# Performance work log

Hardware: AMD Instinct MI355X
Metric: run time of the kernel (lower is better)

Reference implementation:

```python
import jax, jax.numpy as jnp
import numpy as np

T, E, D = 16384, 16, 2048
CAPACITY = 2048  # per-expert capacity (supported_capacities=[2048])
TOP_K = 2


def setup_inputs() -> dict:
    key = jax.random.key(0)
    k1, k2, k3 = jax.random.split(key, 3)
    in_flow = jax.random.normal(k1, (T, D), dtype=jnp.float32)
    # router scores and a realistic top-k multi-hot mask
    logits = jax.random.normal(k2, (T, E), dtype=jnp.float32)
    score = jax.nn.softmax(logits, axis=-1)
    _, topk_idx = jax.lax.top_k(logits, TOP_K)  # [T, TOP_K]
    hot_mask = jnp.zeros((T, E), jnp.int32).at[jnp.arange(T)[:, None], topk_idx].set(1)
    return {"in_flow": in_flow, "hot_mask": hot_mask, "score": score}


def reference(in_flow, hot_mask, score):
    """Capacity-based fused MoE dispatch (HomoFusedDispatchSF):
    1) per-expert local indices via column-wise cumsum of the multi-hot mask,
    2) capacity-clipped loads,
    3) gather tokens scaled by gate score into expert-local buffers [E*C, D].
    """
    hm = (hot_mask > 0).astype(jnp.int32)               # [T, E]
    local = jnp.cumsum(hm, axis=0) * hm                 # 1-based local index per (token, expert)
    loads = jnp.minimum(hm.sum(axis=0), CAPACITY)       # [E]
    pos = local - 1                                     # 0-based slot within expert buffer
    valid = (hm > 0) & (pos < CAPACITY)                 # capacity overflow -> token dropped
    sentinel = E * CAPACITY
    dst = jnp.where(valid, jnp.arange(E)[None, :] * CAPACITY + pos, sentinel).reshape(-1)  # [T*E]
    tok = jnp.broadcast_to(jnp.arange(T, dtype=jnp.int32)[:, None], (T, E)).reshape(-1)
    # invert the scatter: which source token feeds each output slot (T = empty)
    src_tok = jnp.full((sentinel + 1,), T, jnp.int32).at[dst].set(tok)[:sentinel]          # [E*C]
    gate = jnp.zeros((sentinel + 1,), score.dtype).at[dst].set(score.reshape(-1))[:sentinel]
    slot_valid = src_tok < T
    gathered = jnp.take(in_flow, jnp.minimum(src_tok, T - 1), axis=0)                      # [E*C, D]
    out = jnp.where(slot_valid[:, None], gathered * gate[:, None], jnp.zeros((), in_flow.dtype))
    return out, loads
```

## Files before the change

### kernel.cpp

```cpp
#include <hip/hip_runtime.h>

#define T_TOK 16384
#define E_EXP 16
#define CAP   2048
#define D_DIM 2048
#define NCHUNK (T_TOK / 256)
#define NZERO  128

typedef float vf4 __attribute__((ext_vector_type(4)));

__global__ __launch_bounds__(256) void count_kernel(
    const int* __restrict__ hot_mask,
    int*       __restrict__ counts)
{
    const int chunk = blockIdx.x;
    const int tid   = threadIdx.x;
    const int t     = chunk * 256 + tid;
    const int lane  = tid & 63;
    const int wv    = tid >> 6;

    const int4* row = (const int4*)(hot_mask + (size_t)t * E_EXP);
    int4 r0 = row[0], r1 = row[1], r2 = row[2], r3 = row[3];
    int hm[16] = { r0.x > 0, r0.y > 0, r0.z > 0, r0.w > 0,
                   r1.x > 0, r1.y > 0, r1.z > 0, r1.w > 0,
                   r2.x > 0, r2.y > 0, r2.z > 0, r2.w > 0,
                   r3.x > 0, r3.y > 0, r3.z > 0, r3.w > 0 };

    __shared__ int wcnt[4][16];
    #pragma unroll
    for (int e = 0; e < 16; ++e) {
        unsigned long long m = __ballot(hm[e]);
        if (lane == 0) wcnt[wv][e] = __popcll(m);
    }
    __syncthreads();
    if (tid < 16)
        counts[chunk * E_EXP + tid] =
            wcnt[0][tid] + wcnt[1][tid] + wcnt[2][tid] + wcnt[3][tid];
}

__global__ __launch_bounds__(256) void scanfill_kernel(
    const int*   __restrict__ hot_mask,
    const float* __restrict__ score,
    const int*   __restrict__ counts,
    int*         __restrict__ dst2,
    float*       __restrict__ g2,
    int*         __restrict__ loads_i,
    float*       __restrict__ loads_out)
{
    const int chunk = blockIdx.x;
    const int tid   = threadIdx.x;
    const int t     = chunk * 256 + tid;
    const int lane  = tid & 63;
    const int wv    = tid >> 6;

    __shared__ int s_off[16];
    __shared__ int wcnt[4][16];

    if (tid < 16) {
        const int e = tid;
        int off = 0, tot = 0;
        #pragma unroll 8
        for (int c = 0; c < NCHUNK; ++c) {
            const int v = counts[c * E_EXP + e];
            off += (c < chunk) ? v : 0;
            tot += v;
        }
        s_off[e] = off;
        if (chunk == 0) {
            const int ld = tot < CAP ? tot : CAP;
            loads_i[e]   = ld;
            loads_out[e] = (float)ld;
        }
    }

    const int4* mrow = (const int4*)(hot_mask + (size_t)t * E_EXP);
    int4 r0 = mrow[0], r1 = mrow[1], r2 = mrow[2], r3 = mrow[3];
    int hm[16] = { r0.x > 0, r0.y > 0, r0.z > 0, r0.w > 0,
                   r1.x > 0, r1.y > 0, r1.z > 0, r1.w > 0,
                   r2.x > 0, r2.y > 0, r2.z > 0, r2.w > 0,
                   r3.x > 0, r3.y > 0, r3.z > 0, r3.w > 0 };

    const float4* srow = (const float4*)(score + (size_t)t * E_EXP);
    float4 s0 = srow[0], s1 = srow[1], s2 = srow[2], s3 = srow[3];
    float sc[16] = { s0.x, s0.y, s0.z, s0.w, s1.x, s1.y, s1.z, s1.w,
                     s2.x, s2.y, s2.z, s2.w, s3.x, s3.y, s3.z, s3.w };

    int before[16];
    const unsigned long long lmask = (1ULL << lane) - 1ULL;
    #pragma unroll
    for (int e = 0; e < 16; ++e) {
        unsigned long long m = __ballot(hm[e]);
        before[e] = __popcll(m & lmask);
        if (lane == 0) wcnt[wv][e] = __popcll(m);
    }
    __syncthreads();

    int   d0 = -1, d1 = -1;
    float gg0 = 0.f, gg1 = 0.f;
    int   k = 0;
    #pragma unroll
    for (int e = 0; e < 16; ++e) {
        if (hm[e]) {
            int woff = 0;
            for (int w = 0; w < 4; ++w) if (w < wv) woff += wcnt[w][e];
            const int pos  = s_off[e] + woff + before[e];
            const int slot = (pos < CAP) ? e * CAP + pos : -1;
            if (k == 0)      { d0 = slot; gg0 = sc[e]; }
            else if (k == 1) { d1 = slot; gg1 = sc[e]; }
            ++k;
        }
    }
    ((int2*)dst2)[t]  = make_int2(d0, d1);
    ((float2*)g2)[t]  = make_float2(gg0, gg1);
}

__global__ __launch_bounds__(256) void gather_kernel(
    const float* __restrict__ in_flow,
    const int*   __restrict__ dst2,
    const float* __restrict__ g2,
    const int*   __restrict__ loads_i,
    float*       __restrict__ out)
{
    const int b   = blockIdx.x;
    const int tid = threadIdx.x;

    if (b < NZERO) {
        const int e = b >> 3, p = b & 7;
        const int ld = loads_i[e];
        const vf4 z = {0.f, 0.f, 0.f, 0.f};
        for (int s = ld + p; s < CAP; s += 8) {
            vf4* o = (vf4*)(out + ((size_t)e * CAP + s) * D_DIM);
            __builtin_nontemporal_store(z, o + tid);
            __builtin_nontemporal_store(z, o + tid + 256);
        }
        return;
    }

    const int t  = b - NZERO;
    const int d0 = dst2[2 * t];
    const int d1 = dst2[2 * t + 1];
    if (d0 < 0 && d1 < 0) return;

    const vf4* irow = (const vf4*)(in_flow + (size_t)t * D_DIM);
    vf4 v0 = __builtin_nontemporal_load(irow + tid);
    vf4 v1 = __builtin_nontemporal_load(irow + tid + 256);

    if (d0 >= 0) {
        const float g = g2[2 * t];
        vf4* o = (vf4*)(out + (size_t)d0 * D_DIM);
        __builtin_nontemporal_store(v0 * g, o + tid);
        __builtin_nontemporal_store(v1 * g, o + tid + 256);
    }
    if (d1 >= 0) {
        const float g = g2[2 * t + 1];
        vf4* o = (vf4*)(out + (size_t)d1 * D_DIM);
        __builtin_nontemporal_store(v0 * g, o + tid);
        __builtin_nontemporal_store(v1 * g, o + tid + 256);
    }
}

extern "C" void kernel_launch(void* const* d_in, const int* in_sizes, int n_in,
                              void* d_out, int out_size, void* d_ws, size_t ws_size,
                              hipStream_t stream) {
    const float* in_flow  = (const float*)d_in[0];
    const int*   hot_mask = (const int*)d_in[1];
    const float* score    = (const float*)d_in[2];

    float* out       = (float*)d_out;
    float* loads_out = out + (size_t)E_EXP * CAP * D_DIM;

    char* ws = (char*)d_ws;
    int*   counts  = (int*)ws;   ws += NCHUNK * E_EXP * sizeof(int);
    int*   loads_i = (int*)ws;   ws += 64 * sizeof(int);
    int*   dst2    = (int*)ws;   ws += (size_t)T_TOK * 2 * sizeof(int);
    float* g2      = (float*)ws;

    count_kernel<<<NCHUNK, 256, 0, stream>>>(hot_mask, counts);
    scanfill_kernel<<<NCHUNK, 256, 0, stream>>>(hot_mask, score, counts,
                                                dst2, g2, loads_i, loads_out);
    gather_kernel<<<T_TOK + NZERO, 256, 0, stream>>>(in_flow, dst2, g2,
                                                     loads_i, out);
}
```

Baseline: 362.9 us.

## Fuse count, scan and gather into one cooperative kernel with grid sync

Replaces the three-kernel pipeline (count, scan/fill, gather) with a single cooperative kernel of 1024 blocks, each handling 16 tokens. Blocks publish per-expert counts, synchronize across the grid, compute prefix offsets locally, then gather and scale their tokens and zero unused slots. This removes two kernel launches and the round-trip of destination and gate arrays through global memory. In exchange it adds a grid-wide barrier, and each block now walks 16 rows serially, which may reduce memory-level parallelism compared with one block per token.

```diff
diff --git a/kernel.cpp b/kernel.cpp
--- a/kernel.cpp
+++ b/kernel.cpp
@@ -1,161 +1,131 @@
 #include <hip/hip_runtime.h>
+#include <hip/hip_cooperative_groups.h>
+
+namespace cg = cooperative_groups;
 
 #define T_TOK 16384
 #define E_EXP 16
 #define CAP   2048
 #define D_DIM 2048
-#define NCHUNK (T_TOK / 256)
-#define NZERO  128
+#define NBLK  1024
+#define TPB   16
+#define NZERO 128
 
 typedef float vf4 __attribute__((ext_vector_type(4)));
 
-__global__ __launch_bounds__(256) void count_kernel(
-    const int* __restrict__ hot_mask,
-    int*       __restrict__ counts)
-{
-    const int chunk = blockIdx.x;
-    const int tid   = threadIdx.x;
-    const int t     = chunk * 256 + tid;
-    const int lane  = tid & 63;
-    const int wv    = tid >> 6;
-
-    const int4* row = (const int4*)(hot_mask + (size_t)t * E_EXP);
-    int4 r0 = row[0], r1 = row[1], r2 = row[2], r3 = row[3];
-    int hm[16] = { r0.x > 0, r0.y > 0, r0.z > 0, r0.w > 0,
-                   r1.x > 0, r1.y > 0, r1.z > 0, r1.w > 0,
-                   r2.x > 0, r2.y > 0, r2.z > 0, r2.w > 0,
-                   r3.x > 0, r3.y > 0, r3.z > 0, r3.w > 0 };
-
-    __shared__ int wcnt[4][16];
-    #pragma unroll
-    for (int e = 0; e < 16; ++e) {
-        unsigned long long m = __ballot(hm[e]);
-        if (lane == 0) wcnt[wv][e] = __popcll(m);
-    }
-    __syncthreads();
-    if (tid < 16)
-        counts[chunk * E_EXP + tid] =
-            wcnt[0][tid] + wcnt[1][tid] + wcnt[2][tid] + wcnt[3][tid];
-}
-
-__global__ __launch_bounds__(256) void scanfill_kernel(
+__global__ __launch_bounds__(256, 4) void fused_kernel(
+    const float* __restrict__ in_flow,
     const int*   __restrict__ hot_mask,
     const float* __restrict__ score,
-    const int*   __restrict__ counts,
-    int*         __restrict__ dst2,
-    float*       __restrict__ g2,
-    int*         __restrict__ loads_i,
-    float*       __restrict__ loads_out)
-{
-    const int chunk = blockIdx.x;
-    const int tid   = threadIdx.x;
-    const int t     = chunk * 256 + tid;
-    const int lane  = tid & 63;
-    const int wv    = tid >> 6;
-
-    __shared__ int s_off[16];
-    __shared__ int wcnt[4][16];
-
-    if (tid < 16) {
-        const int e = tid;
-        int off = 0, tot = 0;
-        #pragma unroll 8
-        for (int c = 0; c < NCHUNK; ++c) {
-            const int v = counts[c * E_EXP + e];
-            off += (c < chunk) ? v : 0;
-            tot += v;
-        }
-        s_off[e] = off;
-        if (chunk == 0) {
-            const int ld = tot < CAP ? tot : CAP;
-            loads_i[e]   = ld;
-            loads_out[e] = (float)ld;
-        }
-    }
-
-    const int4* mrow = (const int4*)(hot_mask + (size_t)t * E_EXP);
-    int4 r0 = mrow[0], r1 = mrow[1], r2 = mrow[2], r3 = mrow[3];
-    int hm[16] = { r0.x > 0, r0.y > 0, r0.z > 0, r0.w > 0,
-                   r1.x > 0, r1.y > 0, r1.z > 0, r1.w > 0,
-                   r2.x > 0, r2.y > 0, r2.z > 0, r2.w > 0,
-                   r3.x > 0, r3.y > 0, r3.z > 0, r3.w > 0 };
-
-    const float4* srow = (const float4*)(score + (size_t)t * E_EXP);
-    float4 s0 = srow[0], s1 = srow[1], s2 = srow[2], s3 = srow[3];
-    float sc[16] = { s0.x, s0.y, s0.z, s0.w, s1.x, s1.y, s1.z, s1.w,
-                     s2.x, s2.y, s2.z, s2.w, s3.x, s3.y, s3.z, s3.w };
-
-    int before[16];
-    const unsigned long long lmask = (1ULL << lane) - 1ULL;
-    #pragma unroll
-    for (int e = 0; e < 16; ++e) {
-        unsigned long long m = __ballot(hm[e]);
-        before[e] = __popcll(m & lmask);
-        if (lane == 0) wcnt[wv][e] = __popcll(m);
-    }
-    __syncthreads();
-
-    int   d0 = -1, d1 = -1;
-    float gg0 = 0.f, gg1 = 0.f;
-    int   k = 0;
-    #pragma unroll
-    for (int e = 0; e < 16; ++e) {
-        if (hm[e]) {
-            int woff = 0;
-            for (int w = 0; w < 4; ++w) if (w < wv) woff += wcnt[w][e];
-            const int pos  = s_off[e] + woff + before[e];
-            const int slot = (pos < CAP) ? e * CAP + pos : -1;
-            if (k == 0)      { d0 = slot; gg0 = sc[e]; }
-            else if (k == 1) { d1 = slot; gg1 = sc[e]; }
-            ++k;
-        }
-    }
-    ((int2*)dst2)[t]  = make_int2(d0, d1);
-    ((float2*)g2)[t]  = make_float2(gg0, gg1);
-}
-
-__global__ __launch_bounds__(256) void gather_kernel(
-    const float* __restrict__ in_flow,
-    const int*   __restrict__ dst2,
-    const float* __restrict__ g2,
-    const int*   __restrict__ loads_i,
+    int*         __restrict__ counts_T,
+    float*       __restrict__ loads_out,
     float*       __restrict__ out)
 {
     const int b   = blockIdx.x;
     const int tid = threadIdx.x;
 
+    __shared__ int   s_hm[TPB][E_EXP + 1];
+    __shared__ int   s_mask[E_EXP];
+    __shared__ int   s_part_pref[E_EXP][17];
+    __shared__ int   s_part_tot [E_EXP][17];
+    __shared__ int   s_co[E_EXP];
+    __shared__ int   s_tot[E_EXP];
+    __shared__ int   s_dst[TPB][2];
+    __shared__ float s_g[TPB][2];
+
+    s_hm[tid >> 4][tid & 15] = hot_mask[b * 256 + tid] > 0;
+    __syncthreads();
+    if (tid < E_EXP) {
+        int m = 0;
+        #pragma unroll
+        for (int tl = 0; tl < TPB; ++tl) m |= s_hm[tl][tid] << tl;
+        s_mask[tid] = m;
+        counts_T[tid * NBLK + b] = __popc(m);
+    }
+
+    cg::this_grid().sync();
+
+    {
+        const int e   = tid >> 4;
+        const int seg = tid & 15;
+        const int* ce = counts_T + e * NBLK;
+        int pref = 0, tot = 0;
+        #pragma unroll 4
+        for (int c = seg; c < NBLK; c += 16) {
+            const int v = ce[c];
+            tot  += v;
+            pref += (c < b) ? v : 0;
+        }
+        s_part_pref[e][seg] = pref;
+        s_part_tot [e][seg] = tot;
+    }
+    __syncthreads();
+    if (tid < E_EXP) {
+        int pref = 0, tot = 0;
+        #pragma unroll
+        for (int s = 0; s < 16; ++s) {
+            pref += s_part_pref[tid][s];
+            tot  += s_part_tot [tid][s];
+        }
+        s_co[tid]  = pref;
+        s_tot[tid] = tot;
+        if (b == 0) loads_out[tid] = (float)(tot < CAP ? tot : CAP);
+    }
+    __syncthreads();
+
+    if (tid < TPB) {
+        const int tl = tid;
+        const int t  = b * TPB + tl;
+        int   d0 = -1, d1 = -1;
+        float g0 = 0.f, g1 = 0.f;
+        int   k = 0;
+        #pragma unroll
+        for (int e = 0; e < E_EXP; ++e) {
+            const int m = s_mask[e];
+            if ((m >> tl) & 1) {
+                const int pos  = s_co[e] + __popc(m & ((1 << tl) - 1));
+                const int slot = (pos < CAP) ? e * CAP + pos : -1;
+                const float sc = score[t * E_EXP + e];
+                if (k == 0)      { d0 = slot; g0 = sc; }
+                else if (k == 1) { d1 = slot; g1 = sc; }
+                ++k;
+            }
+        }
+        s_dst[tl][0] = d0; s_dst[tl][1] = d1;
+        s_g[tl][0]   = g0; s_g[tl][1]   = g1;
+    }
+    __syncthreads();
+
+    for (int tl = 0; tl < TPB; ++tl) {
+        const int d0 = s_dst[tl][0];
+        const int d1 = s_dst[tl][1];
+        if (d0 < 0 && d1 < 0) continue;
+        const vf4* irow = (const vf4*)(in_flow + (size_t)(b * TPB + tl) * D_DIM);
+        const vf4 v0 = __builtin_nontemporal_load(irow + tid);
+        const vf4 v1 = __builtin_nontemporal_load(irow + tid + 256);
+        if (d0 >= 0) {
+            const float g = s_g[tl][0];
+            vf4* o = (vf4*)(out + (size_t)d0 * D_DIM);
+            __builtin_nontemporal_store(v0 * g, o + tid);
+            __builtin_nontemporal_store(v1 * g, o + tid + 256);
+        }
+        if (d1 >= 0) {
+            const float g = s_g[tl][1];
+            vf4* o = (vf4*)(out + (size_t)d1 * D_DIM);
+            __builtin_nontemporal_store(v0 * g, o + tid);
+            __builtin_nontemporal_store(v1 * g, o + tid + 256);
+        }
+    }
+
     if (b < NZERO) {
-        const int e = b >> 3, p = b & 7;
-        const int ld = loads_i[e];
+        const int e  = b >> 3, p = b & 7;
+        const int ld = min(s_tot[e], CAP);
         const vf4 z = {0.f, 0.f, 0.f, 0.f};
         for (int s = ld + p; s < CAP; s += 8) {
             vf4* o = (vf4*)(out + ((size_t)e * CAP + s) * D_DIM);
             __builtin_nontemporal_store(z, o + tid);
             __builtin_nontemporal_store(z, o + tid + 256);
         }
-        return;
-    }
-
-    const int t  = b - NZERO;
-    const int d0 = dst2[2 * t];
-    const int d1 = dst2[2 * t + 1];
-    if (d0 < 0 && d1 < 0) return;
-
-    const vf4* irow = (const vf4*)(in_flow + (size_t)t * D_DIM);
-    vf4 v0 = __builtin_nontemporal_load(irow + tid);
-    vf4 v1 = __builtin_nontemporal_load(irow + tid + 256);
-
-    if (d0 >= 0) {
-        const float g = g2[2 * t];
-        vf4* o = (vf4*)(out + (size_t)d0 * D_DIM);
-        __builtin_nontemporal_store(v0 * g, o + tid);
-        __builtin_nontemporal_store(v1 * g, o + tid + 256);
-    }
-    if (d1 >= 0) {
-        const float g = g2[2 * t + 1];
-        vf4* o = (vf4*)(out + (size_t)d1 * D_DIM);
-        __builtin_nontemporal_store(v0 * g, o + tid);
-        __builtin_nontemporal_store(v1 * g, o + tid + 256);
     }
 }
 
@@ -169,15 +139,10 @@
     float* out       = (float*)d_out;
     float* loads_out = out + (size_t)E_EXP * CAP * D_DIM;
 
-    char* ws = (char*)d_ws;
-    int*   counts  = (int*)ws;   ws += NCHUNK * E_EXP * sizeof(int);
-    int*   loads_i = (int*)ws;   ws += 64 * sizeof(int);
-    int*   dst2    = (int*)ws;   ws += (size_t)T_TOK * 2 * sizeof(int);
-    float* g2      = (float*)ws;
+    int* counts_T = (int*)d_ws;
 
-    count_kernel<<<NCHUNK, 256, 0, stream>>>(hot_mask, counts);
-    scanfill_kernel<<<NCHUNK, 256, 0, stream>>>(hot_mask, score, counts,
-                                                dst2, g2, loads_i, loads_out);
-    gather_kernel<<<T_TOK + NZERO, 256, 0, stream>>>(in_flow, dst2, g2,
-                                                     loads_i, out);
+    void* args[] = { (void*)&in_flow, (void*)&hot_mask, (void*)&score,
+                     (void*)&counts_T, (void*)&loads_out, (void*)&out };
+    hipLaunchCooperativeKernel(reinterpret_cast<void*>(fused_kernel),
+                               dim3(NBLK), dim3(256), args, 0, stream);
 }
```

Measured after the change: 444.5 us. 22.5% more time.
